# Kernel tuning notes

Hardware: AMD Instinct MI355X
Metric: run time of the kernel (lower is better)

## Reference

```python
import jax, jax.numpy as jnp
import numpy as np

N_NODES = 50000
NNZ = 800000
HYPER_DIM = 128
N_LAYERS = 2
LEAKY = 0.2
LN_EPS = 1e-5


def setup_inputs() -> dict:
    key = jax.random.key(0)
    k1, k2, k3, k4 = jax.random.split(key, 4)
    return {
        "ego_embeddings": jax.random.normal(k1, (N_NODES, HYPER_DIM), dtype=jnp.float32),
        "adj_vals": jax.random.uniform(k2, (NNZ,), dtype=jnp.float32),
        "ln_gamma": jnp.ones((N_LAYERS, HYPER_DIM), dtype=jnp.float32),
        "ln_beta": jnp.zeros((N_LAYERS, HYPER_DIM), dtype=jnp.float32),
        "adj_rows": jax.random.randint(k3, (NNZ,), 0, N_NODES, dtype=jnp.int32),
        "adj_cols": jax.random.randint(k4, (NNZ,), 0, N_NODES, dtype=jnp.int32),
        "n_users": 25000,
    }


def _spmm(rows, cols, vals, x, n_out):
    # y = A @ x for sparse A in COO (rows, cols, vals): gather + segment-sum
    return jax.ops.segment_sum(vals[:, None] * x[cols], rows, num_segments=n_out)


def _layer_norm(x, gamma, beta):
    mu = jnp.mean(x, axis=-1, keepdims=True)
    var = jnp.mean(jnp.square(x - mu), axis=-1, keepdims=True)
    return (x - mu) * jax.lax.rsqrt(var + LN_EPS) * gamma + beta


def reference(ego_embeddings, adj_vals, ln_gamma, ln_beta, adj_rows, adj_cols, n_users):
    res = ego_embeddings
    embs = ego_embeddings
    for k in range(N_LAYERS):
        # adj.T @ embs  (rows of A^T are cols of A)
        ht = _spmm(adj_cols, adj_rows, adj_vals, embs, N_NODES)
        # adj @ (adj.T @ embs)
        h = _spmm(adj_rows, adj_cols, adj_vals, ht, N_NODES)
        if k != N_LAYERS - 1:
            h = jnp.where(h >= 0, h, LEAKY * h)  # LeakyReLU
        embs = _layer_norm(h, ln_gamma[k], ln_beta[k]) + res
    user_emb = embs[:n_users]
    item_emb = embs[n_users:]
    return (user_emb, item_emb)
```

## Files before the change

### kernel.cpp

```cpp
#include <hip/hip_runtime.h>
#include <hip/hip_bf16.h>

#define HD 128
#define PB 256
#define LEAKY 0.2f
#define LN_EPS 1e-5f

__device__ __forceinline__ unsigned short bfr(float f) {
    unsigned int b = __float_as_uint(f);
    return (unsigned short)((b + 0x7fffu + ((b >> 16) & 1u)) >> 16);
}
__device__ __forceinline__ float blo(unsigned int u) { return __uint_as_float(u << 16); }
__device__ __forceinline__ float bhi(unsigned int u) { return __uint_as_float(u & 0xffff0000u); }


__global__ __launch_bounds__(256) void part_count(
    const int* __restrict__ rows, const int* __restrict__ cols,
    int* __restrict__ counts,
    const float* __restrict__ ego, unsigned short* __restrict__ ego_bf,
    int nnz, int n4) {
    __shared__ int cR[64], cC[64];
    if (threadIdx.x < 64) { cR[threadIdx.x] = 0; cC[threadIdx.x] = 0; }
    __syncthreads();
    int chunk = (nnz + PB - 1) / PB;
    int beg = blockIdx.x * chunk;
    int end = min(beg + chunk, nnz);
    for (int i = beg + threadIdx.x; i < end; i += 256) {
        atomicAdd(&cR[rows[i] >> 10], 1);
        atomicAdd(&cC[cols[i] >> 10], 1);
    }
    for (int i = blockIdx.x * 256 + threadIdx.x; i < n4; i += 256 * PB) {
        float4 f = ((const float4*)ego)[i];
        ushort4 u;
        u.x = bfr(f.x); u.y = bfr(f.y); u.z = bfr(f.z); u.w = bfr(f.w);
        ((ushort4*)ego_bf)[i] = u;
    }
    __syncthreads();
    if (threadIdx.x < 64) {
        counts[(size_t)blockIdx.x * 64 + threadIdx.x] = cR[threadIdx.x];
        counts[(size_t)PB * 64 + blockIdx.x * 64 + threadIdx.x] = cC[threadIdx.x];
    }
}

__global__ __launch_bounds__(64) void part_off(
    int* __restrict__ counts, int* __restrict__ totals) {
    int bkt = blockIdx.x, dir = blockIdx.y, lane = threadIdx.x;
    int* p = counts + (size_t)dir * PB * 64;
    int v[4], s = 0;
    #pragma unroll
    for (int j = 0; j < 4; ++j) {
        int blk = lane * 4 + j;
        v[j] = p[(size_t)blk * 64 + bkt];
        s += v[j];
    }
    int incl = s;
    #pragma unroll
    for (int off = 1; off < 64; off <<= 1) {
        int t = __shfl_up(incl, off);
        if (lane >= off) incl += t;
    }
    int excl = incl - s;
    #pragma unroll
    for (int j = 0; j < 4; ++j) {
        int blk = lane * 4 + j;
        p[(size_t)blk * 64 + bkt] = excl;
        excl += v[j];
    }
    if (lane == 63) totals[dir * 64 + bkt] = incl;
}

__global__ __launch_bounds__(256) void part_scatter(
    const int* __restrict__ rows, const int* __restrict__ cols,
    const float* __restrict__ vals,
    const int* __restrict__ counts, const int* __restrict__ totals,
    uint2* __restrict__ stg_r, uint2* __restrict__ stg_c, int nnz, int nbk) {
    __shared__ int cR[64], cC[64], wbR[64], wbC[64];
    if (threadIdx.x < 64) {
        int t = threadIdx.x;
        cR[t] = 0; cC[t] = 0;
        int vR = (t < nbk) ? totals[t] : 0;
        int vC = (t < nbk) ? totals[64 + t] : 0;
        int iR = vR, iC = vC;
        #pragma unroll
        for (int off = 1; off < 64; off <<= 1) {
            int a = __shfl_up(iR, off), b = __shfl_up(iC, off);
            if (t >= off) { iR += a; iC += b; }
        }
        wbR[t] = iR - vR + counts[(size_t)blockIdx.x * 64 + t];
        wbC[t] = iC - vC + counts[(size_t)PB * 64 + blockIdx.x * 64 + t];
    }
    __syncthreads();
    int chunk = (nnz + PB - 1) / PB;
    int beg = blockIdx.x * chunk;
    int end = min(beg + chunk, nnz);
    for (int i = beg + threadIdx.x; i < end; i += 256) {
        int ro = rows[i], co = cols[i];
        unsigned vb = (unsigned)bfr(vals[i]) << 16;
        int rk = atomicAdd(&cR[ro >> 10], 1);
        stg_r[wbR[ro >> 10] + rk] = make_uint2(vb | (unsigned)co, (unsigned)ro);
        int ck = atomicAdd(&cC[co >> 10], 1);
        stg_c[wbC[co >> 10] + ck] = make_uint2(vb | (unsigned)ro, (unsigned)co);
    }
}

__global__ __launch_bounds__(1024) void bucket_build(
    const uint2* __restrict__ stg_r, const uint2* __restrict__ stg_c,
    const int* __restrict__ totals,
    unsigned* __restrict__ ent_r, unsigned* __restrict__ ent_c,
    int* __restrict__ rp_r, int* __restrict__ rp_c, int n, int nnz) {
    __shared__ int cnt[1024];
    __shared__ int wsum[16], woff[16];
    __shared__ int s_base;
    int bkt = blockIdx.x, dir = blockIdx.y;
    const uint2* stg = dir ? stg_c : stg_r;
    unsigned* ent = dir ? ent_c : ent_r;
    int* rp = dir ? rp_c : rp_r;
    if (threadIdx.x < 64) {
        int v = (threadIdx.x < bkt) ? totals[dir * 64 + threadIdx.x] : 0;
        #pragma unroll
        for (int off = 32; off; off >>= 1) v += __shfl_xor(v, off);
        if (threadIdx.x == 0) s_base = v;
    }
    cnt[threadIdx.x] = 0;
    __syncthreads();
    int base = s_base;
    int total = totals[dir * 64 + bkt];
    int lo = bkt << 10;
    int nb = min(1024, n - lo);
    for (int i = threadIdx.x; i < total; i += 1024)
        atomicAdd(&cnt[(int)stg[base + i].y - lo], 1);
    __syncthreads();
    int lane = threadIdx.x & 63, wid = threadIdx.x >> 6;
    int v = cnt[threadIdx.x];
    int incl = v;
    #pragma unroll
    for (int off = 1; off < 64; off <<= 1) {
        int t = __shfl_up(incl, off);
        if (lane >= off) incl += t;
    }
    if (lane == 63) wsum[wid] = incl;
    __syncthreads();
    if (threadIdx.x == 0) {
        int run = 0;
        #pragma unroll
        for (int w = 0; w < 16; ++w) { woff[w] = run; run += wsum[w]; }
    }
    __syncthreads();
    int excl = woff[wid] + incl - v;
    if (threadIdx.x < nb) rp[lo + threadIdx.x] = base + excl;
    if (bkt == gridDim.x - 1 && threadIdx.x == 0) rp[n] = nnz;
    cnt[threadIdx.x] = excl;
    __syncthreads();
    for (int i = threadIdx.x; i < total; i += 1024) {
        uint2 e = stg[base + i];
        int pos = atomicAdd(&cnt[(int)e.y - lo], 1);
        ent[base + pos] = e.x;
    }
}

__global__ __launch_bounds__(256) void spmm_bf(
    const unsigned short* __restrict__ x, const int* __restrict__ rp,
    const unsigned* __restrict__ ent,
    const unsigned short* __restrict__ res, const float* __restrict__ gamma,
    const float* __restrict__ beta,
    unsigned short* __restrict__ out_bf, float* __restrict__ out_f32,
    int n, int post) {
    int wid = threadIdx.x >> 6, lane = threadIdx.x & 63;
    int row = blockIdx.x * 4 + wid;
    if (row >= n) return;
    int quarter = lane >> 4, q = lane & 15;
    int beg = rp[row], end = rp[row + 1];
    float acc[8];
    #pragma unroll
    for (int k = 0; k < 8; ++k) acc[k] = 0.f;

    int i = beg + quarter;
    for (; i + 12 < end; i += 16) {
        unsigned e0 = ent[i], e1 = ent[i + 4], e2 = ent[i + 8], e3 = ent[i + 12];
        uint4 u0 = ((const uint4*)(x + (size_t)(e0 & 0xffffu) * HD))[q];
        uint4 u1 = ((const uint4*)(x + (size_t)(e1 & 0xffffu) * HD))[q];
        uint4 u2 = ((const uint4*)(x + (size_t)(e2 & 0xffffu) * HD))[q];
        uint4 u3 = ((const uint4*)(x + (size_t)(e3 & 0xffffu) * HD))[q];
        float v0 = bhi(e0), v1 = bhi(e1), v2 = bhi(e2), v3 = bhi(e3);
        acc[0] += v0 * blo(u0.x) + v1 * blo(u1.x);
        acc[1] += v0 * bhi(u0.x) + v1 * bhi(u1.x);
        acc[2] += v0 * blo(u0.y) + v1 * blo(u1.y);
        acc[3] += v0 * bhi(u0.y) + v1 * bhi(u1.y);
        acc[4] += v0 * blo(u0.z) + v1 * blo(u1.z);
        acc[5] += v0 * bhi(u0.z) + v1 * bhi(u1.z);
        acc[6] += v0 * blo(u0.w) + v1 * blo(u1.w);
        acc[7] += v0 * bhi(u0.w) + v1 * bhi(u1.w);
        acc[0] += v2 * blo(u2.x) + v3 * blo(u3.x);
        acc[1] += v2 * bhi(u2.x) + v3 * bhi(u3.x);
        acc[2] += v2 * blo(u2.y) + v3 * blo(u3.y);
        acc[3] += v2 * bhi(u2.y) + v3 * bhi(u3.y);
        acc[4] += v2 * blo(u2.z) + v3 * blo(u3.z);
        acc[5] += v2 * bhi(u2.z) + v3 * bhi(u3.z);
        acc[6] += v2 * blo(u2.w) + v3 * blo(u3.w);
        acc[7] += v2 * bhi(u2.w) + v3 * bhi(u3.w);
    }
    for (; i < end; i += 4) {
        unsigned e0 = ent[i];
        uint4 u0 = ((const uint4*)(x + (size_t)(e0 & 0xffffu) * HD))[q];
        float v0 = bhi(e0);
        acc[0] += v0 * blo(u0.x);
        acc[1] += v0 * bhi(u0.x);
        acc[2] += v0 * blo(u0.y);
        acc[3] += v0 * bhi(u0.y);
        acc[4] += v0 * blo(u0.z);
        acc[5] += v0 * bhi(u0.z);
        acc[6] += v0 * blo(u0.w);
        acc[7] += v0 * bhi(u0.w);
    }
    #pragma unroll
    for (int k = 0; k < 8; ++k) {
        acc[k] += __shfl_xor(acc[k], 16);
        acc[k] += __shfl_xor(acc[k], 32);
    }
    if (quarter != 0) return;

    if (post == 0) {
        uint4 s;
        s.x = (unsigned)bfr(acc[0]) | ((unsigned)bfr(acc[1]) << 16);
        s.y = (unsigned)bfr(acc[2]) | ((unsigned)bfr(acc[3]) << 16);
        s.z = (unsigned)bfr(acc[4]) | ((unsigned)bfr(acc[5]) << 16);
        s.w = (unsigned)bfr(acc[6]) | ((unsigned)bfr(acc[7]) << 16);
        ((uint4*)(out_bf + (size_t)row * HD))[q] = s;
        return;
    }
    if (post == 1) {
        #pragma unroll
        for (int k = 0; k < 8; ++k) acc[k] = acc[k] >= 0.f ? acc[k] : LEAKY * acc[k];
    }
    float t = 0.f;
    #pragma unroll
    for (int k = 0; k < 8; ++k) t += acc[k];
    #pragma unroll
    for (int off = 1; off < 16; off <<= 1) t += __shfl_xor(t, off);
    float mu = t * (1.f / HD);
    float d[8], vs = 0.f;
    #pragma unroll
    for (int k = 0; k < 8; ++k) { d[k] = acc[k] - mu; vs += d[k] * d[k]; }
    #pragma unroll
    for (int off = 1; off < 16; off <<= 1) vs += __shfl_xor(vs, off);
    float inv = rsqrtf(vs * (1.f / HD) + LN_EPS);

    float4 g0 = ((const float4*)gamma)[2 * q], g1 = ((const float4*)gamma)[2 * q + 1];
    float4 b0 = ((const float4*)beta)[2 * q],  b1 = ((const float4*)beta)[2 * q + 1];
    uint4 ru = ((const uint4*)(res + (size_t)row * HD))[q];
    float o[8];
    o[0] = d[0] * inv * g0.x + b0.x + blo(ru.x);
    o[1] = d[1] * inv * g0.y + b0.y + bhi(ru.x);
    o[2] = d[2] * inv * g0.z + b0.z + blo(ru.y);
    o[3] = d[3] * inv * g0.w + b0.w + bhi(ru.y);
    o[4] = d[4] * inv * g1.x + b1.x + blo(ru.z);
    o[5] = d[5] * inv * g1.y + b1.y + bhi(ru.z);
    o[6] = d[6] * inv * g1.z + b1.z + blo(ru.w);
    o[7] = d[7] * inv * g1.w + b1.w + bhi(ru.w);
    if (post == 1) {
        uint4 s;
        s.x = (unsigned)bfr(o[0]) | ((unsigned)bfr(o[1]) << 16);
        s.y = (unsigned)bfr(o[2]) | ((unsigned)bfr(o[3]) << 16);
        s.z = (unsigned)bfr(o[4]) | ((unsigned)bfr(o[5]) << 16);
        s.w = (unsigned)bfr(o[6]) | ((unsigned)bfr(o[7]) << 16);
        ((uint4*)(out_bf + (size_t)row * HD))[q] = s;
    } else {
        float4 s0 = {o[0], o[1], o[2], o[3]};
        float4 s1 = {o[4], o[5], o[6], o[7]};
        ((float4*)(out_f32 + (size_t)row * HD))[2 * q] = s0;
        ((float4*)(out_f32 + (size_t)row * HD))[2 * q + 1] = s1;
    }
}

extern "C" void kernel_launch(void* const* d_in, const int* in_sizes, int n_in,
                              void* d_out, int out_size, void* d_ws, size_t ws_size,
                              hipStream_t stream) {
    const float* ego   = (const float*)d_in[0];
    const float* vals  = (const float*)d_in[1];
    const float* gamma = (const float*)d_in[2];
    const float* beta  = (const float*)d_in[3];
    const int*   rows  = (const int*)d_in[4];
    const int*   cols  = (const int*)d_in[5];

    const int N   = in_sizes[0] / HD;
    const int NNZ = in_sizes[1];
    const int NBK = (N + 1023) >> 10;

    float* out = (float*)d_out;
    char* w = (char*)d_ws;
    unsigned short* ego_bf = (unsigned short*)w; w += (size_t)N * HD * 2;
    unsigned short* bufA   = (unsigned short*)w; w += (size_t)N * HD * 2;
    unsigned short* bufB   = (unsigned short*)w; w += (size_t)N * HD * 2;
    int*  rp_r = (int*)w;  w += (size_t)(N + 4) * 4;
    int*  rp_c = (int*)w;  w += (size_t)(N + 4) * 4;
    unsigned* ent_r = (unsigned*)w; w += (size_t)NNZ * 4;
    unsigned* ent_c = (unsigned*)w; w += (size_t)NNZ * 4;
    int* counts = (int*)w; w += (size_t)2 * PB * 64 * 4;
    int* totals = (int*)w; w += 128 * 4;

    uint2* stg_r = (uint2*)bufB;
    uint2* stg_c = stg_r + NNZ;

    part_count<<<PB, 256, 0, stream>>>(rows, cols, counts, ego, ego_bf,
                                       NNZ, N * HD / 4);
    part_off<<<dim3(NBK, 2), 64, 0, stream>>>(counts, totals);
    part_scatter<<<PB, 256, 0, stream>>>(rows, cols, vals, counts, totals,
                                         stg_r, stg_c, NNZ, NBK);
    bucket_build<<<dim3(NBK, 2), 1024, 0, stream>>>(stg_r, stg_c, totals,
                                                    ent_r, ent_c, rp_r, rp_c,
                                                    N, NNZ);

    const int sblocks = (N + 3) / 4;

    spmm_bf<<<sblocks, 256, 0, stream>>>(ego_bf, rp_c, ent_c,
                                         nullptr, nullptr, nullptr, bufA, nullptr, N, 0);
    spmm_bf<<<sblocks, 256, 0, stream>>>(bufA, rp_r, ent_r,
                                         ego_bf, gamma, beta, bufB, nullptr, N, 1);
    spmm_bf<<<sblocks, 256, 0, stream>>>(bufB, rp_c, ent_c,
                                         nullptr, nullptr, nullptr, bufA, nullptr, N, 0);
    spmm_bf<<<sblocks, 256, 0, stream>>>(bufA, rp_r, ent_r,
                                         ego_bf, gamma + HD, beta + HD, nullptr, out, N, 2);
}
```

Baseline: 268.1 us.

## Fuse partition count and scatter using global atomic cursors into fixed-capacity buckets

Replaces the three-kernel partition pipeline (count, offset scan, scatter) with one kernel. Each block counts its bucket hits, then reserves space with global atomics into fixed-capacity per-bucket regions (CAP entries). Bin indices are kept as separate 16-bit arrays instead of 8-byte staging pairs, which cuts staging traffic and two launches. The cost is a memset, extra workspace, and a fixed CAP that assumes no 1024-node bucket exceeds 20480 entries. That holds for uniform random indices but would overflow silently on skewed graphs.

Result: no change. 272.9 us (+1.8%).

```diff
diff --git a/kernel.cpp b/kernel.cpp
--- a/kernel.cpp
+++ b/kernel.cpp
@@ -2,7 +2,8 @@
 #include <hip/hip_bf16.h>
 
 #define HD 128
-#define PB 256
+#define PB 512
+#define CAP 20480
 #define LEAKY 0.2f
 #define LN_EPS 1e-5f
 
@@ -13,13 +14,15 @@
 __device__ __forceinline__ float blo(unsigned int u) { return __uint_as_float(u << 16); }
 __device__ __forceinline__ float bhi(unsigned int u) { return __uint_as_float(u & 0xffff0000u); }
 
-
-__global__ __launch_bounds__(256) void part_count(
+__global__ __launch_bounds__(256) void scatter_direct(
     const int* __restrict__ rows, const int* __restrict__ cols,
-    int* __restrict__ counts,
+    const float* __restrict__ vals,
     const float* __restrict__ ego, unsigned short* __restrict__ ego_bf,
+    int* __restrict__ gcur,
+    unsigned* __restrict__ pay_r, unsigned short* __restrict__ bin_r,
+    unsigned* __restrict__ pay_c, unsigned short* __restrict__ bin_c,
     int nnz, int n4) {
-    __shared__ int cR[64], cC[64];
+    __shared__ int cR[64], cC[64], wbR[64], wbC[64];
     if (threadIdx.x < 64) { cR[threadIdx.x] = 0; cC[threadIdx.x] = 0; }
     __syncthreads();
     int chunk = (nnz + PB - 1) / PB;
@@ -37,86 +40,45 @@
     }
     __syncthreads();
     if (threadIdx.x < 64) {
-        counts[(size_t)blockIdx.x * 64 + threadIdx.x] = cR[threadIdx.x];
-        counts[(size_t)PB * 64 + blockIdx.x * 64 + threadIdx.x] = cC[threadIdx.x];
-    }
-}
-
-__global__ __launch_bounds__(64) void part_off(
-    int* __restrict__ counts, int* __restrict__ totals) {
-    int bkt = blockIdx.x, dir = blockIdx.y, lane = threadIdx.x;
-    int* p = counts + (size_t)dir * PB * 64;
-    int v[4], s = 0;
-    #pragma unroll
-    for (int j = 0; j < 4; ++j) {
-        int blk = lane * 4 + j;
-        v[j] = p[(size_t)blk * 64 + bkt];
-        s += v[j];
-    }
-    int incl = s;
-    #pragma unroll
-    for (int off = 1; off < 64; off <<= 1) {
-        int t = __shfl_up(incl, off);
-        if (lane >= off) incl += t;
-    }
-    int excl = incl - s;
-    #pragma unroll
-    for (int j = 0; j < 4; ++j) {
-        int blk = lane * 4 + j;
-        p[(size_t)blk * 64 + bkt] = excl;
-        excl += v[j];
-    }
-    if (lane == 63) totals[dir * 64 + bkt] = incl;
-}
-
-__global__ __launch_bounds__(256) void part_scatter(
-    const int* __restrict__ rows, const int* __restrict__ cols,
-    const float* __restrict__ vals,
-    const int* __restrict__ counts, const int* __restrict__ totals,
-    uint2* __restrict__ stg_r, uint2* __restrict__ stg_c, int nnz, int nbk) {
-    __shared__ int cR[64], cC[64], wbR[64], wbC[64];
-    if (threadIdx.x < 64) {
         int t = threadIdx.x;
+        wbR[t] = cR[t] ? atomicAdd(&gcur[t], cR[t]) : 0;
+        wbC[t] = cC[t] ? atomicAdd(&gcur[64 + t], cC[t]) : 0;
         cR[t] = 0; cC[t] = 0;
-        int vR = (t < nbk) ? totals[t] : 0;
-        int vC = (t < nbk) ? totals[64 + t] : 0;
-        int iR = vR, iC = vC;
-        #pragma unroll
-        for (int off = 1; off < 64; off <<= 1) {
-            int a = __shfl_up(iR, off), b = __shfl_up(iC, off);
-            if (t >= off) { iR += a; iC += b; }
-        }
-        wbR[t] = iR - vR + counts[(size_t)blockIdx.x * 64 + t];
-        wbC[t] = iC - vC + counts[(size_t)PB * 64 + blockIdx.x * 64 + t];
-    }
-    __syncthreads();
-    int chunk = (nnz + PB - 1) / PB;
-    int beg = blockIdx.x * chunk;
-    int end = min(beg + chunk, nnz);
+    }
+    __syncthreads();
     for (int i = beg + threadIdx.x; i < end; i += 256) {
         int ro = rows[i], co = cols[i];
         unsigned vb = (unsigned)bfr(vals[i]) << 16;
-        int rk = atomicAdd(&cR[ro >> 10], 1);
-        stg_r[wbR[ro >> 10] + rk] = make_uint2(vb | (unsigned)co, (unsigned)ro);
-        int ck = atomicAdd(&cC[co >> 10], 1);
-        stg_c[wbC[co >> 10] + ck] = make_uint2(vb | (unsigned)ro, (unsigned)co);
+        int bk = ro >> 10;
+        int rk = atomicAdd(&cR[bk], 1);
+        int idx = bk * CAP + wbR[bk] + rk;
+        pay_r[idx] = vb | (unsigned)co;
+        bin_r[idx] = (unsigned short)(ro & 1023);
+        bk = co >> 10;
+        rk = atomicAdd(&cC[bk], 1);
+        idx = bk * CAP + wbC[bk] + rk;
+        pay_c[idx] = vb | (unsigned)ro;
+        bin_c[idx] = (unsigned short)(co & 1023);
     }
 }
 
 __global__ __launch_bounds__(1024) void bucket_build(
-    const uint2* __restrict__ stg_r, const uint2* __restrict__ stg_c,
-    const int* __restrict__ totals,
+    const unsigned* __restrict__ pay_r, const unsigned short* __restrict__ bin_r,
+    const unsigned* __restrict__ pay_c, const unsigned short* __restrict__ bin_c,
+    const int* __restrict__ gcur,
     unsigned* __restrict__ ent_r, unsigned* __restrict__ ent_c,
-    int* __restrict__ rp_r, int* __restrict__ rp_c, int n, int nnz) {
+    int* __restrict__ rp_r, int* __restrict__ rp_c,
+    int n, int nnz, int nbk) {
     __shared__ int cnt[1024];
     __shared__ int wsum[16], woff[16];
     __shared__ int s_base;
     int bkt = blockIdx.x, dir = blockIdx.y;
-    const uint2* stg = dir ? stg_c : stg_r;
+    const unsigned* pay = dir ? pay_c : pay_r;
+    const unsigned short* bin = dir ? bin_c : bin_r;
     unsigned* ent = dir ? ent_c : ent_r;
     int* rp = dir ? rp_c : rp_r;
     if (threadIdx.x < 64) {
-        int v = (threadIdx.x < bkt) ? totals[dir * 64 + threadIdx.x] : 0;
+        int v = (threadIdx.x < bkt) ? gcur[dir * 64 + threadIdx.x] : 0;
         #pragma unroll
         for (int off = 32; off; off >>= 1) v += __shfl_xor(v, off);
         if (threadIdx.x == 0) s_base = v;
@@ -124,11 +86,13 @@
     cnt[threadIdx.x] = 0;
     __syncthreads();
     int base = s_base;
-    int total = totals[dir * 64 + bkt];
+    int total = gcur[dir * 64 + bkt];
     int lo = bkt << 10;
     int nb = min(1024, n - lo);
+    const unsigned short* bb = bin + (size_t)bkt * CAP;
+    const unsigned* pb = pay + (size_t)bkt * CAP;
     for (int i = threadIdx.x; i < total; i += 1024)
-        atomicAdd(&cnt[(int)stg[base + i].y - lo], 1);
+        atomicAdd(&cnt[bb[i]], 1);
     __syncthreads();
     int lane = threadIdx.x & 63, wid = threadIdx.x >> 6;
     int v = cnt[threadIdx.x];
@@ -148,13 +112,12 @@
     __syncthreads();
     int excl = woff[wid] + incl - v;
     if (threadIdx.x < nb) rp[lo + threadIdx.x] = base + excl;
-    if (bkt == gridDim.x - 1 && threadIdx.x == 0) rp[n] = nnz;
+    if (bkt == nbk - 1 && threadIdx.x == 0) rp[n] = nnz;
     cnt[threadIdx.x] = excl;
     __syncthreads();
     for (int i = threadIdx.x; i < total; i += 1024) {
-        uint2 e = stg[base + i];
-        int pos = atomicAdd(&cnt[(int)e.y - lo], 1);
-        ent[base + pos] = e.x;
+        int pos = atomicAdd(&cnt[bb[i]], 1);
+        ent[base + pos] = pb[i];
     }
 }
 
@@ -291,24 +254,23 @@
     unsigned short* ego_bf = (unsigned short*)w; w += (size_t)N * HD * 2;
     unsigned short* bufA   = (unsigned short*)w; w += (size_t)N * HD * 2;
     unsigned short* bufB   = (unsigned short*)w; w += (size_t)N * HD * 2;
-    int*  rp_r = (int*)w;  w += (size_t)(N + 4) * 4;
-    int*  rp_c = (int*)w;  w += (size_t)(N + 4) * 4;
+    int*  rp_r = (int*)w;  w += (size_t)(N + 8) * 4;
+    int*  rp_c = (int*)w;  w += (size_t)(N + 8) * 4;
     unsigned* ent_r = (unsigned*)w; w += (size_t)NNZ * 4;
     unsigned* ent_c = (unsigned*)w; w += (size_t)NNZ * 4;
-    int* counts = (int*)w; w += (size_t)2 * PB * 64 * 4;
-    int* totals = (int*)w; w += 128 * 4;
-
-    uint2* stg_r = (uint2*)bufB;
-    uint2* stg_c = stg_r + NNZ;
-
-    part_count<<<PB, 256, 0, stream>>>(rows, cols, counts, ego, ego_bf,
-                                       NNZ, N * HD / 4);
-    part_off<<<dim3(NBK, 2), 64, 0, stream>>>(counts, totals);
-    part_scatter<<<PB, 256, 0, stream>>>(rows, cols, vals, counts, totals,
-                                         stg_r, stg_c, NNZ, NBK);
-    bucket_build<<<dim3(NBK, 2), 1024, 0, stream>>>(stg_r, stg_c, totals,
-                                                    ent_r, ent_c, rp_r, rp_c,
-                                                    N, NNZ);
+    unsigned* pay_r = (unsigned*)w; w += (size_t)64 * CAP * 4;
+    unsigned* pay_c = (unsigned*)w; w += (size_t)64 * CAP * 4;
+    unsigned short* bin_r = (unsigned short*)w; w += (size_t)64 * CAP * 2;
+    unsigned short* bin_c = (unsigned short*)w; w += (size_t)64 * CAP * 2;
+    int* gcur = (int*)w; w += 128 * 4;
+
+    hipMemsetAsync(gcur, 0, 128 * 4, stream);
+    scatter_direct<<<PB, 256, 0, stream>>>(rows, cols, vals, ego, ego_bf, gcur,
+                                           pay_r, bin_r, pay_c, bin_c,
+                                           NNZ, N * HD / 4);
+    bucket_build<<<dim3(NBK, 2), 1024, 0, stream>>>(pay_r, bin_r, pay_c, bin_c,
+                                                    gcur, ent_r, ent_c,
+                                                    rp_r, rp_c, N, NNZ, NBK);
 
     const int sblocks = (N + 3) / 4;
 
```
